# Performance work log

Measured on AMD Instinct MI355X. Metric: run time of the kernel, lower is better.

## Reference

```python
import jax, jax.numpy as jnp
import numpy as np

D_MODEL = 1024
N_HEADS = 16
D_K = 64
B = 2
S = 2048


def setup_inputs() -> dict:
    key = jax.random.key(0)
    ks = jax.random.split(key, 6)
    scale = 1.0 / np.sqrt(D_MODEL)
    x = jax.random.normal(ks[0], (B, S, D_MODEL), dtype=jnp.float32)
    Wq = jax.random.normal(ks[1], (D_MODEL, D_MODEL), dtype=jnp.float32) * scale
    Wk = jax.random.normal(ks[2], (D_MODEL, D_MODEL), dtype=jnp.float32) * scale
    Wv = jax.random.normal(ks[3], (D_MODEL, D_MODEL), dtype=jnp.float32) * scale
    Wo = jax.random.normal(ks[4], (D_MODEL, D_MODEL), dtype=jnp.float32) * scale
    bq = jnp.zeros((D_MODEL,), jnp.float32)
    bk = jnp.zeros((D_MODEL,), jnp.float32)
    bv = jnp.zeros((D_MODEL,), jnp.float32)
    bo = jnp.zeros((D_MODEL,), jnp.float32)
    # causal mask, broadcast over batch and heads: [1, 1, S, S]
    mask = jnp.tril(jnp.ones((S, S), jnp.int32))[None, None, :, :]
    return {"x": x, "mask": mask, "Wq": Wq, "bq": bq, "Wk": Wk, "bk": bk,
            "Wv": Wv, "bv": bv, "Wo": Wo, "bo": bo}


def reference(x, mask, Wq, bq, Wk, bk, Wv, bv, Wo, bo):
    b, s, _ = x.shape
    # projections (torch Linear: y = x @ W^T + b); split heads -> [b, h, s, d_k]
    def split_heads(y):
        return y.reshape(b, s, N_HEADS, D_K).transpose(0, 2, 1, 3)
    Q = split_heads(x @ Wq.T + bq)
    K = split_heads(x @ Wk.T + bk)
    V = split_heads(x @ Wv.T + bv)
    scores = jnp.einsum('bhqd,bhkd->bhqk', Q, K) / jnp.sqrt(jnp.float32(D_K))
    scores = jnp.where(mask == 0, -jnp.inf, scores)
    attn = jax.nn.softmax(scores, axis=-1)  # dropout p=0 -> identity
    out = jnp.einsum('bhqk,bhkd->bhqd', attn, V)
    out = out.transpose(0, 2, 1, 3).reshape(b, s, D_MODEL)
    return out @ Wo.T + bo
```

## Files before the change

kernel.cpp:

```cpp
#include <hip/hip_runtime.h>
#include <math.h>
#include <type_traits>

#define D_MODEL 1024
#define N_HEADS 16
#define D_KK    64
#define B_SZ    2
#define SEQ     2048
#define M_TOTAL (B_SZ * SEQ)

#define QSCALE 0.18033688011112042f

typedef __attribute__((ext_vector_type(8))) short short8;
typedef __attribute__((ext_vector_type(4))) float f32x4;

static __device__ __forceinline__ ushort f2bf(float f) {
    union { float f; unsigned u; } c; c.f = f;
    unsigned u = c.u;
    unsigned r = (u + 0x7fffu + ((u >> 16) & 1u)) >> 16;
    return (ushort)r;
}

static __device__ __forceinline__ unsigned packbf(float a, float b) {
    unsigned ua = __float_as_uint(a) + 0x8000u;
    unsigned ub = __float_as_uint(b) + 0x8000u;
    return __builtin_amdgcn_perm(ub, ua, 0x07060302u);
}

static __device__ __forceinline__ void gload16(const void* g, void* l) {
    __builtin_amdgcn_global_load_lds(
        (const __attribute__((address_space(1))) void*)g,
        (__attribute__((address_space(3))) void*)l, 16, 0, 0);
}

__global__ __launch_bounds__(256)
void cvt_kernel(const float* __restrict__ x,  const float* __restrict__ wq,
                const float* __restrict__ wk, const float* __restrict__ wv,
                const float* __restrict__ wo,
                ushort* __restrict__ xb,  ushort* __restrict__ wqb,
                ushort* __restrict__ wkb, ushort* __restrict__ wvb,
                ushort* __restrict__ wob)
{
    const float* s; ushort* d; int n4;
    switch (blockIdx.y) {
        case 0:  s = x;  d = xb;  n4 = M_TOTAL * D_MODEL / 4; break;
        case 1:  s = wq; d = wqb; n4 = D_MODEL * D_MODEL / 4; break;
        case 2:  s = wk; d = wkb; n4 = D_MODEL * D_MODEL / 4; break;
        case 3:  s = wv; d = wvb; n4 = D_MODEL * D_MODEL / 4; break;
        default: s = wo; d = wob; n4 = D_MODEL * D_MODEL / 4; break;
    }
    const int stride = gridDim.x * blockDim.x;
    for (int i = blockIdx.x * blockDim.x + threadIdx.x; i < n4; i += stride) {
        float4 v = reinterpret_cast<const float4*>(s)[i];
        ushort4 u;
        u.x = f2bf(v.x); u.y = f2bf(v.y); u.z = f2bf(v.z); u.w = f2bf(v.w);
        reinterpret_cast<ushort4*>(d)[i] = u;
    }
}

template<int EPI>
__global__ __launch_bounds__(256)
void gemm_mfma(const ushort* __restrict__ A,
               const ushort* __restrict__ W0, const float* __restrict__ b0, void* __restrict__ C0,
               const ushort* __restrict__ W1, const float* __restrict__ b1, void* __restrict__ C1,
               const ushort* __restrict__ W2, const float* __restrict__ b2, void* __restrict__ C2)
{
    constexpr int K = D_MODEL;

    __shared__ ushort As[2][128 * 64];
    __shared__ ushort Bs[2][64 * 64];

    const int id  = blockIdx.x;
    const int xcd = id & 7;
    const int j   = id >> 3;
    const int mt  = xcd * 4 + (j & 3);
    const int ntz = j >> 2;
    const int nt  = ntz & 15;
    const int z   = ntz >> 4;

    const ushort* W    = W0;
    const float*  bias = b0;
    void*         C    = C0;
    if (z == 1) { W = W1; bias = b1; C = C1; }
    else if (z == 2) { W = W2; bias = b2; C = C2; }

    const int m0 = mt * 128;
    const int n0 = nt * 64;

    const int tid  = threadIdx.x;
    const int w    = tid >> 6;
    const int lane = tid & 63;
    const int lr   = lane & 15;
    const int lc   = lane >> 4;
    const int wr   = w >> 1;
    const int wc   = w & 1;

    const int rsub = lane >> 3;
    const int csw  = ((lane & 7) ^ rsub) << 3;

    const ushort* gA = A + (size_t)(m0 + w * 8 + rsub) * K + csw;
    const ushort* gB = W + (size_t)(n0 + w * 8 + rsub) * K + csw;

    f32x4 acc[4][2];
#pragma unroll
    for (int m = 0; m < 4; ++m)
#pragma unroll
        for (int n = 0; n < 2; ++n) acc[m][n] = (f32x4)0.0f;

#pragma unroll
    for (int ca = 0; ca < 4; ++ca)
        gload16(gA + (size_t)(32 * ca) * K, &As[0][(w + 4 * ca) * 512]);
#pragma unroll
    for (int cb = 0; cb < 2; ++cb)
        gload16(gB + (size_t)(32 * cb) * K, &Bs[0][(w + 4 * cb) * 512]);
    __syncthreads();

    const int swz = (lr & 7) << 4;
    int buf = 0;
    for (int it = 0; it < 16; ++it) {
        if (it < 15) {
            const int kn = (it + 1) * 64;
#pragma unroll
            for (int ca = 0; ca < 4; ++ca)
                gload16(gA + (size_t)(32 * ca) * K + kn, &As[buf ^ 1][(w + 4 * ca) * 512]);
#pragma unroll
            for (int cb = 0; cb < 2; ++cb)
                gload16(gB + (size_t)(32 * cb) * K + kn, &Bs[buf ^ 1][(w + 4 * cb) * 512]);
        }

        short8 af[4][2], bfr[2][2];
#pragma unroll
        for (int m = 0; m < 4; ++m) {
            const int rbyte = (wr * 64 + m * 16 + lr) * 128;
#pragma unroll
            for (int kk = 0; kk < 2; ++kk)
                af[m][kk] = *reinterpret_cast<const short8*>(
                    &As[buf][(rbyte + ((kk * 64 + lc * 16) ^ swz)) >> 1]);
        }
#pragma unroll
        for (int n = 0; n < 2; ++n) {
            const int rbyte = (wc * 32 + n * 16 + lr) * 128;
#pragma unroll
            for (int kk = 0; kk < 2; ++kk)
                bfr[n][kk] = *reinterpret_cast<const short8*>(
                    &Bs[buf][(rbyte + ((kk * 64 + lc * 16) ^ swz)) >> 1]);
        }
#pragma unroll
        for (int kk = 0; kk < 2; ++kk)
#pragma unroll
            for (int m = 0; m < 4; ++m)
#pragma unroll
                for (int n = 0; n < 2; ++n)
                    acc[m][n] = __builtin_amdgcn_mfma_f32_16x16x32_bf16(
                        af[m][kk], bfr[n][kk], acc[m][n], 0, 0, 0);

        __syncthreads();
        buf ^= 1;
    }

    float bv[2];
#pragma unroll
    for (int n = 0; n < 2; ++n) bv[n] = bias[n0 + wc * 32 + n * 16 + lr];
    const int row_base = m0 + wr * 64;

    if (EPI == 0) {
        float* Cf = (float*)C;
#pragma unroll
        for (int m = 0; m < 4; ++m)
#pragma unroll
        for (int r = 0; r < 4; ++r) {
            const int row = row_base + m * 16 + lc * 4 + r;
#pragma unroll
            for (int n = 0; n < 2; ++n)
                Cf[(size_t)row * D_MODEL + n0 + wc * 32 + n * 16 + lr] =
                    acc[m][n][r] + bv[n];
        }
    } else {
        ushort* Cu = (ushort*)C;
        const bool vt   = (z == 2);
        const float osc = (z == 0) ? QSCALE : 1.0f;
#pragma unroll
        for (int m = 0; m < 4; ++m) {
            const int row4 = row_base + m * 16 + lc * 4;
            const int bb = row4 >> 11;
            const int ss = row4 & 2047;
            const size_t bhbase = (size_t)bb * N_HEADS;
#pragma unroll
            for (int n = 0; n < 2; ++n) {
                const int col = n0 + wc * 32 + n * 16 + lr;
                const int h = col >> 6, d = col & 63;
                if (vt) {
                    ushort4 u;
                    u.x = f2bf(acc[m][n][0] + bv[n]);
                    u.y = f2bf(acc[m][n][1] + bv[n]);
                    u.z = f2bf(acc[m][n][2] + bv[n]);
                    u.w = f2bf(acc[m][n][3] + bv[n]);
                    *reinterpret_cast<ushort4*>(
                        &Cu[((bhbase + h) * D_KK + d) * SEQ + ss]) = u;
                } else {
#pragma unroll
                    for (int r = 0; r < 4; ++r)
                        Cu[((bhbase + h) * SEQ + ss + r) * D_KK + d] =
                            f2bf((acc[m][n][r] + bv[n]) * osc);
                }
            }
        }
    }
}

__global__ __launch_bounds__(256, 4)
void attn_mfma_kernel(const ushort* __restrict__ Qb, const ushort* __restrict__ Kb,
                      const ushort* __restrict__ Vt, ushort* __restrict__ Ob)
{
    __shared__ ushort Ks[2][4096];
    __shared__ ushort Vs[2][4096];
    __shared__ ushort P_lds[4][1024];

    const int tid  = threadIdx.x;
    const int w    = tid >> 6;
    const int lane = tid & 63;
    const int lr   = lane & 15;
    const int lc   = lane >> 4;

    const int id  = blockIdx.x;
    const int xcd = id & 7;
    const int j   = id >> 3;
    const int bh  = xcd * 4 + (j & 3);
    const int qx  = j >> 2;
    const int b   = bh >> 4;
    const int h   = bh & 15;

    const ushort* Kbase = Kb + (size_t)bh * SEQ * D_KK;
    const ushort* Vbase = Vt + (size_t)bh * D_KK * SEQ;

    const int rsub = lane >> 3;
    const int csw  = ((lane & 7) ^ rsub) << 3;

    ushort* Pw     = &P_lds[w][0];
    const int sw_w = (lr & 7) << 4;

    for (int half = 0; half < 2; ++half) {
        const int qb  = half ? (31 - qx) : qx;
        const int q0  = qb * 64;
        const int qr0 = q0 + w * 16;
        const int nt  = qb + 1;

        const ushort* Qp = Qb + ((size_t)bh * SEQ + qr0 + lr) * D_KK + lc * 8;
        const short8 qa0 = *reinterpret_cast<const short8*>(Qp);
        const short8 qa1 = *reinterpret_cast<const short8*>(Qp + 32);

        f32x4 acc_o[4];
#pragma unroll
        for (int t = 0; t < 4; ++t) acc_o[t] = (f32x4)0.0f;
        float m_run = -1e30f;
        float l_run = 0.0f;

#pragma unroll
        for (int cc = 0; cc < 2; ++cc) {
            const int c = w + cc * 4;
            gload16(Kbase + (size_t)(c * 8 + rsub) * D_KK + csw, &Ks[0][c * 512]);
            gload16(Vbase + (size_t)(c * 8 + rsub) * SEQ + csw,  &Vs[0][c * 512]);
        }
        __syncthreads();

        auto tile_body = [&](int buf, auto maskc) {
            constexpr bool MASK = decltype(maskc)::value;
            const ushort* Ksb = &Ks[buf][0];
            const ushort* Vsb = &Vs[buf][0];

            f32x4 s[4];
#pragma unroll
            for (int t = 0; t < 4; ++t) {
                const int rbyte = (t * 16 + lr) * 128;
                const short8 kb0 = *reinterpret_cast<const short8*>(
                    &Ksb[(rbyte + ((lc * 16) ^ sw_w)) >> 1]);
                const short8 kb1 = *reinterpret_cast<const short8*>(
                    &Ksb[(rbyte + ((64 + lc * 16) ^ sw_w)) >> 1]);
                f32x4 a = (f32x4)0.0f;
                a = __builtin_amdgcn_mfma_f32_16x16x32_bf16(kb0, qa0, a, 0, 0, 0);
                a = __builtin_amdgcn_mfma_f32_16x16x32_bf16(kb1, qa1, a, 0, 0, 0);
                s[t] = a;
            }

            float tmax = -1e30f;
#pragma unroll
            for (int t = 0; t < 4; ++t)
#pragma unroll
                for (int r = 0; r < 4; ++r) {
                    if (MASK) {
                        const int kl = t * 16 + lc * 4 + r;
                        if (kl > w * 16 + lr) s[t][r] = -1e30f;
                    }
                    tmax = fmaxf(tmax, s[t][r]);
                }
            tmax = fmaxf(tmax, __shfl_xor(tmax, 16));
            tmax = fmaxf(tmax, __shfl_xor(tmax, 32));

            if (!__all(tmax <= m_run + 8.0f)) {
                const float mnew = fmaxf(m_run, tmax);
                const float corr = __builtin_amdgcn_exp2f(m_run - mnew);
                m_run = mnew;
                l_run *= corr;
                float cr[4];
#pragma unroll
                for (int r = 0; r < 4; ++r) cr[r] = __shfl(corr, lc * 4 + r, 16);
#pragma unroll
                for (int t = 0; t < 4; ++t)
#pragma unroll
                    for (int r = 0; r < 4; ++r) acc_o[t][r] *= cr[r];
            }

            float rsum = 0.0f;
#pragma unroll
            for (int t = 0; t < 4; ++t) {
#pragma unroll
                for (int r = 0; r < 4; ++r) {
                    const float p = __builtin_amdgcn_exp2f(s[t][r] - m_run);
                    s[t][r] = p;
                    rsum += p;
                }
                const unsigned lo = packbf(s[t][0], s[t][1]);
                const unsigned hi = packbf(s[t][2], s[t][3]);
                *reinterpret_cast<uint2*>(
                    &Pw[(lr * 128 + ((t * 32 + lc * 8) ^ sw_w)) >> 1]) =
                    make_uint2(lo, hi);
            }
            rsum += __shfl_xor(rsum, 16);
            rsum += __shfl_xor(rsum, 32);
            l_run += rsum;

            const short8 pa0 = *reinterpret_cast<const short8*>(
                &Pw[(lr * 128 + ((lc * 16) ^ sw_w)) >> 1]);
            const short8 pa1 = *reinterpret_cast<const short8*>(
                &Pw[(lr * 128 + ((64 + lc * 16) ^ sw_w)) >> 1]);

#pragma unroll
            for (int t = 0; t < 4; ++t) {
                const int rbyte = (t * 16 + lr) * 128;
                const short8 vb0 = *reinterpret_cast<const short8*>(
                    &Vsb[(rbyte + ((lc * 16) ^ sw_w)) >> 1]);
                const short8 vb1 = *reinterpret_cast<const short8*>(
                    &Vsb[(rbyte + ((64 + lc * 16) ^ sw_w)) >> 1]);
                acc_o[t] = __builtin_amdgcn_mfma_f32_16x16x32_bf16(
                        pa0, vb0, acc_o[t], 0, 0, 0);
                acc_o[t] = __builtin_amdgcn_mfma_f32_16x16x32_bf16(
                        pa1, vb1, acc_o[t], 0, 0, 0);
            }
        };

        int buf = 0;
        for (int it = 0; it < nt - 1; ++it) {
            const int kn = (it + 1) * 64;
#pragma unroll
            for (int cc = 0; cc < 2; ++cc) {
                const int c = w + cc * 4;
                gload16(Kbase + (size_t)(kn + c * 8 + rsub) * D_KK + csw,
                        &Ks[buf ^ 1][c * 512]);
                gload16(Vbase + (size_t)(c * 8 + rsub) * SEQ + kn + csw,
                        &Vs[buf ^ 1][c * 512]);
            }
            tile_body(buf, std::integral_constant<bool, false>{});
            __syncthreads();
            buf ^= 1;
        }
        tile_body(buf, std::integral_constant<bool, true>{});

        const float linv = 1.0f / l_run;
        float invr[4];
#pragma unroll
        for (int r = 0; r < 4; ++r) invr[r] = __shfl(linv, lc * 4 + r, 16);
#pragma unroll
        for (int r = 0; r < 4; ++r) {
            const int qrow = qr0 + lc * 4 + r;
            ushort* Op = Ob + ((size_t)b * SEQ + qrow) * D_MODEL + h * D_KK;
#pragma unroll
            for (int t = 0; t < 4; ++t)
                Op[t * 16 + lr] = f2bf(acc_o[t][r] * invr[r]);
        }

        if (half == 0) __syncthreads();
    }
}

extern "C" void kernel_launch(void* const* d_in, const int* in_sizes, int n_in,
                              void* d_out, int out_size, void* d_ws, size_t ws_size,
                              hipStream_t stream)
{
    const float* x  = (const float*)d_in[0];
    const float* Wq = (const float*)d_in[2];
    const float* bq = (const float*)d_in[3];
    const float* Wk = (const float*)d_in[4];
    const float* bk = (const float*)d_in[5];
    const float* Wv = (const float*)d_in[6];
    const float* bv = (const float*)d_in[7];
    const float* Wo = (const float*)d_in[8];
    const float* bo = (const float*)d_in[9];
    float* out = (float*)d_out;

    const size_t TSZ = (size_t)M_TOTAL * D_MODEL;
    const size_t WSZ = (size_t)D_MODEL * D_MODEL;
    ushort* xb  = (ushort*)d_ws;
    ushort* Wqb = xb  + TSZ;
    ushort* Wkb = Wqb + WSZ;
    ushort* Wvb = Wkb + WSZ;
    ushort* Wob = Wvb + WSZ;
    ushort* Qb  = Wob + WSZ;
    ushort* Kb  = Qb  + TSZ;
    ushort* Vt  = Kb  + TSZ;
    ushort* Ob  = Vt  + TSZ;

    dim3 blk(256);
    cvt_kernel<<<dim3(256, 5), blk, 0, stream>>>(x, Wq, Wk, Wv, Wo,
                                                 xb, Wqb, Wkb, Wvb, Wob);

    gemm_mfma<1><<<dim3(1536), blk, 0, stream>>>(xb, Wqb, bq, Qb,
                                                     Wkb, bk, Kb,
                                                     Wvb, bv, Vt);

    attn_mfma_kernel<<<dim3(512), blk, 0, stream>>>(Qb, Kb, Vt, Ob);

    gemm_mfma<0><<<dim3(512), blk, 0, stream>>>(Ob, Wob, bo, out,
                                                    Wob, bo, out,
                                                    Wob, bo, out);
}
```

Baseline: 106.8 us.

## Triple-buffer K/V tiles in attention with fine-grained vmcnt waits

```diff
diff --git a/kernel.cpp b/kernel.cpp
--- a/kernel.cpp
+++ b/kernel.cpp
@@ -212,8 +212,8 @@
 void attn_mfma_kernel(const ushort* __restrict__ Qb, const ushort* __restrict__ Kb,
                       const ushort* __restrict__ Vt, ushort* __restrict__ Ob)
 {
-    __shared__ ushort Ks[2][4096];
-    __shared__ ushort Vs[2][4096];
+    __shared__ ushort Ks[3][4096];
+    __shared__ ushort Vs[3][4096];
     __shared__ ushort P_lds[4][1024];
 
     const int tid  = threadIdx.x;
@@ -239,6 +239,17 @@
     ushort* Pw     = &P_lds[w][0];
     const int sw_w = (lr & 7) << 4;
 
+    auto stage = [&](int kofs, int s) {
+#pragma unroll
+        for (int cc = 0; cc < 2; ++cc) {
+            const int c = w + cc * 4;
+            gload16(Kbase + (size_t)(kofs + c * 8 + rsub) * D_KK + csw,
+                    &Ks[s][c * 512]);
+            gload16(Vbase + (size_t)(c * 8 + rsub) * SEQ + kofs + csw,
+                    &Vs[s][c * 512]);
+        }
+    };
+
     for (int half = 0; half < 2; ++half) {
         const int qb  = half ? (31 - qx) : qx;
         const int q0  = qb * 64;
@@ -255,18 +266,13 @@
         float m_run = -1e30f;
         float l_run = 0.0f;
 
-#pragma unroll
-        for (int cc = 0; cc < 2; ++cc) {
-            const int c = w + cc * 4;
-            gload16(Kbase + (size_t)(c * 8 + rsub) * D_KK + csw, &Ks[0][c * 512]);
-            gload16(Vbase + (size_t)(c * 8 + rsub) * SEQ + csw,  &Vs[0][c * 512]);
-        }
-        __syncthreads();
-
-        auto tile_body = [&](int buf, auto maskc) {
+        stage(0, 0);
+        if (nt > 1) stage(64, 1);
+
+        auto tile_body = [&](int slot, auto maskc) {
             constexpr bool MASK = decltype(maskc)::value;
-            const ushort* Ksb = &Ks[buf][0];
-            const ushort* Vsb = &Vs[buf][0];
+            const ushort* Ksb = &Ks[slot][0];
+            const ushort* Vsb = &Vs[slot][0];
 
             f32x4 s[4];
 #pragma unroll
@@ -348,22 +354,23 @@
             }
         };
 
-        int buf = 0;
-        for (int it = 0; it < nt - 1; ++it) {
-            const int kn = (it + 1) * 64;
-#pragma unroll
-            for (int cc = 0; cc < 2; ++cc) {
-                const int c = w + cc * 4;
-                gload16(Kbase + (size_t)(kn + c * 8 + rsub) * D_KK + csw,
-                        &Ks[buf ^ 1][c * 512]);
-                gload16(Vbase + (size_t)(c * 8 + rsub) * SEQ + kn + csw,
-                        &Vs[buf ^ 1][c * 512]);
-            }
-            tile_body(buf, std::integral_constant<bool, false>{});
-            __syncthreads();
-            buf ^= 1;
-        }
-        tile_body(buf, std::integral_constant<bool, true>{});
+        int slot = 0;
+        for (int it = 0; it < nt; ++it) {
+            if (it + 1 < nt) {
+                asm volatile("s_waitcnt vmcnt(4)" ::: "memory");
+            } else {
+                asm volatile("s_waitcnt vmcnt(0)" ::: "memory");
+            }
+            __builtin_amdgcn_s_barrier();
+            __builtin_amdgcn_sched_barrier(0);
+            if (it + 2 < nt) stage((it + 2) * 64, (it + 2) % 3);
+
+            if (it == nt - 1)
+                tile_body(slot, std::integral_constant<bool, true>{});
+            else
+                tile_body(slot, std::integral_constant<bool, false>{});
+            slot = (slot == 2) ? 0 : slot + 1;
+        }
 
         const float linv = 1.0f / l_run;
         float invr[4];
@@ -378,7 +385,7 @@
                 Op[t * 16 + lr] = f2bf(acc_o[t][r] * invr[r]);
         }
 
-        if (half == 0) __syncthreads();
+        __syncthreads();
     }
 }
 
```

Measured after the change: 109.1 us. +2.1%, slower.
